# Kernel optimization log

Measured on AMD Instinct MI355X. Metric: run time of the kernel, lower is better.

The kernel has to match this reference:

```python
import jax, jax.numpy as jnp
import numpy as np

N_NODES = 100000
N_EDGES = 640000
IN_DIM, HID_DIM, OUT_DIM = 128, 64, 32


def setup_inputs() -> dict:
    key = jax.random.key(0)
    ks = jax.random.split(key, 8)
    x = jax.random.normal(ks[0], (N_NODES, IN_DIM), dtype=jnp.float32)
    edge_index = jax.random.randint(ks[1], (2, N_EDGES), 0, N_NODES, dtype=jnp.int64)
    # SAGEConv params: lin_l (applied to aggregated neighbors, has bias),
    # lin_r (applied to root node, no bias) -- PyG defaults.
    s1 = 1.0 / np.sqrt(IN_DIM)
    s2 = 1.0 / np.sqrt(HID_DIM)
    W1l = jax.random.uniform(ks[2], (HID_DIM, IN_DIM), jnp.float32, -s1, s1)
    b1 = jax.random.uniform(ks[3], (HID_DIM,), jnp.float32, -s1, s1)
    W1r = jax.random.uniform(ks[4], (HID_DIM, IN_DIM), jnp.float32, -s1, s1)
    W2l = jax.random.uniform(ks[5], (OUT_DIM, HID_DIM), jnp.float32, -s2, s2)
    b2 = jax.random.uniform(ks[6], (OUT_DIM,), jnp.float32, -s2, s2)
    W2r = jax.random.uniform(ks[7], (OUT_DIM, HID_DIM), jnp.float32, -s2, s2)
    return {"x": x, "edge_index": edge_index,
            "W1l": W1l, "b1": b1, "W1r": W1r,
            "W2l": W2l, "b2": b2, "W2r": W2r}


def _sage_conv(x, src, dst, Wl, b, Wr, num_nodes):
    # mean aggregation of source features onto destination nodes
    msg = x[src]                                                # [E, d]
    agg = jax.ops.segment_sum(msg, dst, num_segments=num_nodes)  # [N, d]
    cnt = jax.ops.segment_sum(jnp.ones((src.shape[0],), x.dtype), dst,
                              num_segments=num_nodes)            # [N]
    agg = agg / jnp.maximum(cnt, 1.0)[:, None]
    # out = lin_l(mean_neighbors) + lin_r(x)
    return agg @ Wl.T + b + x @ Wr.T


def reference(x, edge_index, W1l, b1, W1r, W2l, b2, W2r):
    src, dst = edge_index[0], edge_index[1]
    n = x.shape[0]
    h = jax.nn.relu(_sage_conv(x, src, dst, W1l, b1, W1r, n))
    out = _sage_conv(h, src, dst, W2l, b2, W2r, n)
    return out
```

## Files before the change

kernel.cpp:

```cpp
#include <hip/hip_runtime.h>
#include <hip/hip_bf16.h>

typedef __hip_bfloat16 bf16;
typedef __attribute__((ext_vector_type(8))) short short8;
typedef __attribute__((ext_vector_type(4))) float f32x4;

#define N_NODES 100000
#define N_EDGES 640000
#define NSB 98
#define N_TILES 6250

__device__ __forceinline__ int detect_is64(const int* __restrict__ idx) {
    int lane = threadIdx.x & 63;
    int v = idx[2 * (lane & 31) + 1];
    return __ballot(v == 0) == ~0ULL;
}
__device__ __forceinline__ int detect_f32(const unsigned* __restrict__ xw) {
    int lane = threadIdx.x & 63;
    unsigned e = (xw[lane] >> 7) & 0xFFu;
    int inr = (e >= 0x20u && e <= 0x4Fu);
    return __popcll(__ballot(inr)) < 48;
}

__device__ __forceinline__ void decode8(
        const int* __restrict__ eidx, int is64, int e0, int E,
        int (&ss)[8], int (&dd)[8]) {
    if (is64) {
        int4 a0 = *(const int4*)&eidx[2 * e0];
        int4 a1 = *(const int4*)&eidx[2 * e0 + 4];
        int4 a2 = *(const int4*)&eidx[2 * e0 + 8];
        int4 a3 = *(const int4*)&eidx[2 * e0 + 12];
        int4 b0 = *(const int4*)&eidx[2 * (E + e0)];
        int4 b1 = *(const int4*)&eidx[2 * (E + e0) + 4];
        int4 b2 = *(const int4*)&eidx[2 * (E + e0) + 8];
        int4 b3 = *(const int4*)&eidx[2 * (E + e0) + 12];
        ss[0] = a0.x; ss[1] = a0.z; ss[2] = a1.x; ss[3] = a1.z;
        ss[4] = a2.x; ss[5] = a2.z; ss[6] = a3.x; ss[7] = a3.z;
        dd[0] = b0.x; dd[1] = b0.z; dd[2] = b1.x; dd[3] = b1.z;
        dd[4] = b2.x; dd[5] = b2.z; dd[6] = b3.x; dd[7] = b3.z;
    } else {
        int4 s0 = *(const int4*)&eidx[e0];
        int4 s1 = *(const int4*)&eidx[e0 + 4];
        int4 d0 = *(const int4*)&eidx[E + e0];
        int4 d1 = *(const int4*)&eidx[E + e0 + 4];
        ss[0] = s0.x; ss[1] = s0.y; ss[2] = s0.z; ss[3] = s0.w;
        ss[4] = s1.x; ss[5] = s1.y; ss[6] = s1.z; ss[7] = s1.w;
        dd[0] = d0.x; dd[1] = d0.y; dd[2] = d0.z; dd[3] = d0.w;
        dd[4] = d1.x; dd[5] = d1.y; dd[6] = d1.z; dd[7] = d1.w;
    }
}

__global__ __launch_bounds__(256) void hist_kernel(
        const int* __restrict__ eidx, int* __restrict__ deg,
        int* __restrict__ rank, int E, int N) {
    const int is64 = detect_is64(eidx);
    int e0 = (blockIdx.x * 256 + threadIdx.x) * 8;
    if (e0 >= E) return;
    int ss[8], dd[8], rk[8];
    decode8(eidx, is64, e0, E, ss, dd);
#pragma unroll
    for (int c = 0; c < 8; ++c) {
        bool ok = (unsigned)ss[c] < (unsigned)N && (unsigned)dd[c] < (unsigned)N;
        rk[c] = ok ? atomicAdd(&deg[dd[c]], 1) : 0;
    }
    *(int4*)&rank[e0]     = make_int4(rk[0], rk[1], rk[2], rk[3]);
    *(int4*)&rank[e0 + 4] = make_int4(rk[4], rk[5], rk[6], rk[7]);
}

__global__ __launch_bounds__(256) void scan_partial_kernel(
        const int* __restrict__ deg, int* __restrict__ off,
        int* __restrict__ bsum, int N) {
    __shared__ int ss[256];
    const int tid = threadIdx.x, blk = blockIdx.x;
    const int base = blk * 1024 + tid * 4;
    int v[4], s = 0;
    if (base + 3 < N) {
        int4 dv = *(const int4*)&deg[base];
        v[0] = dv.x; v[1] = dv.y; v[2] = dv.z; v[3] = dv.w;
    } else {
#pragma unroll
        for (int c = 0; c < 4; ++c) v[c] = (base + c < N) ? deg[base + c] : 0;
    }
#pragma unroll
    for (int c = 0; c < 4; ++c) s += v[c];
    ss[tid] = s; __syncthreads();
    for (int o = 1; o < 256; o <<= 1) {
        int t = (tid >= o) ? ss[tid - o] : 0;
        __syncthreads();
        ss[tid] += t;
        __syncthreads();
    }
    int run = ss[tid] - s;
    if (tid == 255) bsum[blk] = ss[255];
#pragma unroll
    for (int c = 0; c < 4; ++c) {
        if (base + c < N) off[base + c] = run;
        run += v[c];
    }
}

__global__ void scan_bsum_kernel(int* __restrict__ bsum, int* __restrict__ off, int N) {
    __shared__ int ss[128];
    const int tid = threadIdx.x;
    int v = (tid < NSB) ? bsum[tid] : 0;
    ss[tid] = v; __syncthreads();
    for (int o = 1; o < 128; o <<= 1) {
        int t = (tid >= o) ? ss[tid - o] : 0;
        __syncthreads();
        ss[tid] += t;
        __syncthreads();
    }
    if (tid < NSB) bsum[tid] = ss[tid] - v;
    if (tid == 127) off[N] = ss[127];
}

__global__ __launch_bounds__(256) void scan_add_kernel(
        int* __restrict__ off, const int* __restrict__ bsum, int N) {
    const int blk = blockIdx.x, tid = threadIdx.x;
    const int add = bsum[blk];
    const int base = blk * 1024 + tid * 4;
#pragma unroll
    for (int c = 0; c < 4; ++c) {
        int i = base + c;
        if (i < N) off[i] += add;
    }
}

__global__ __launch_bounds__(256) void fill_kernel(
        const int* __restrict__ eidx, const int* __restrict__ off,
        const int* __restrict__ rank, int* __restrict__ srcs, int E, int N) {
    const int is64 = detect_is64(eidx);
    int e0 = (blockIdx.x * 256 + threadIdx.x) * 8;
    if (e0 >= E) return;
    int ss[8], dd[8];
    decode8(eidx, is64, e0, E, ss, dd);
    int4 r0 = *(const int4*)&rank[e0];
    int4 r1 = *(const int4*)&rank[e0 + 4];
    const int rk[8] = {r0.x, r0.y, r0.z, r0.w, r1.x, r1.y, r1.z, r1.w};
#pragma unroll
    for (int c = 0; c < 8; ++c) {
        if ((unsigned)ss[c] >= (unsigned)N || (unsigned)dd[c] >= (unsigned)N) continue;
        srcs[off[dd[c]] + rk[c]] = ss[c];
    }
}

__global__ __launch_bounds__(256) void gather1_kernel(
        const int* __restrict__ srcs, const int* __restrict__ off,
        const bf16* __restrict__ xl, const bf16* __restrict__ xr,
        const void* __restrict__ b1, bf16* __restrict__ h,
        const unsigned* __restrict__ xdet, int N) {
    const int f32 = detect_f32(xdet);
    const int node = blockIdx.x * 4 + (threadIdx.x >> 6);
    const int lane = threadIdx.x & 63;
    if (node >= N) return;
    const int a = off[node], b = off[node + 1];
    float acc = 0.f;
    for (int base = a; base < b; base += 64) {
        const int cdeg = min(b - base, 64);
        int sv = (lane < cdeg) ? srcs[base + lane] : 0;
        for (int bb = 0; bb < cdeg; bb += 8) {
            float v[8];
#pragma unroll
            for (int t = 0; t < 8; ++t) {
                int idx = bb + t;
                int s = __shfl(sv, idx < cdeg ? idx : 0);
                float val = (float)xl[(size_t)s * 64 + lane];
                v[t] = (idx < cdeg) ? val : 0.f;
            }
            acc += ((v[0] + v[1]) + (v[2] + v[3])) + ((v[4] + v[5]) + (v[6] + v[7]));
        }
    }
    const float bb = f32 ? ((const float*)b1)[lane] : (float)((const bf16*)b1)[lane];
    const float inv = 1.0f / fmaxf((float)(b - a), 1.0f);
    float v = acc * inv + bb + (float)xr[(size_t)node * 64 + lane];
    h[(size_t)node * 64 + lane] = __float2bfloat16(fmaxf(v, 0.0f));
}

__global__ __launch_bounds__(256) void gather2_kernel(
        const int* __restrict__ srcs, const int* __restrict__ off,
        const bf16* __restrict__ hl, const bf16* __restrict__ hr,
        const void* __restrict__ b2, void* __restrict__ out,
        const unsigned* __restrict__ xdet, int N) {
    const int f32 = detect_f32(xdet);
    const int node = blockIdx.x * 4 + (threadIdx.x >> 6);
    const int lane = threadIdx.x & 63;
    if (node >= N) return;
    const int j = lane & 31, half = lane >> 5;
    const int a = off[node], b = off[node + 1];
    float acc = 0.f;
    for (int base = a; base < b; base += 64) {
        const int cdeg = min(b - base, 64);
        int sv = (lane < cdeg) ? srcs[base + lane] : 0;
        for (int bb = 0; bb < cdeg; bb += 8) {
            float v[4];
#pragma unroll
            for (int t = 0; t < 4; ++t) {
                int idx = bb + half + 2 * t;
                int s = __shfl(sv, idx < cdeg ? idx : 0);
                float val = (float)hl[(size_t)s * 32 + j];
                v[t] = (idx < cdeg) ? val : 0.f;
            }
            acc += (v[0] + v[1]) + (v[2] + v[3]);
        }
    }
    acc += __shfl_down(acc, 32);
    if (half == 0) {
        const float bb = f32 ? ((const float*)b2)[j] : (float)((const bf16*)b2)[j];
        const float inv = 1.0f / fmaxf((float)(b - a), 1.0f);
        float v = acc * inv + bb + (float)hr[(size_t)node * 32 + j];
        if (f32) ((float*)out)[(size_t)node * 32 + j] = v;
        else     ((bf16*)out)[(size_t)node * 32 + j] = __float2bfloat16(v);
    }
}

__device__ __forceinline__ short8 load_frag(const void* base, size_t eoff, int f32) {
    if (f32) {
        const float4* p = (const float4*)((const float*)base + eoff);
        const float4 u = p[0], v = p[1];
        short8 r;
        union { bf16 b; short s; } t;
        t.b = __float2bfloat16(u.x); r[0] = t.s;
        t.b = __float2bfloat16(u.y); r[1] = t.s;
        t.b = __float2bfloat16(u.z); r[2] = t.s;
        t.b = __float2bfloat16(u.w); r[3] = t.s;
        t.b = __float2bfloat16(v.x); r[4] = t.s;
        t.b = __float2bfloat16(v.y); r[5] = t.s;
        t.b = __float2bfloat16(v.z); r[6] = t.s;
        t.b = __float2bfloat16(v.w); r[7] = t.s;
        return r;
    }
    return *(const short8*)((const short*)base + eoff);
}

__global__ __launch_bounds__(256) void lin1_kernel(
        const void* __restrict__ x, const void* __restrict__ W1l,
        const void* __restrict__ W1r, bf16* __restrict__ xl,
        bf16* __restrict__ xr) {
    const int f32 = detect_f32((const unsigned*)x);
    __shared__ short wlds[2][16][64][8];

    const int tid = threadIdx.x;
    {
        const int l = tid & 63, fg = tid >> 6;
        const int mm = l & 15, qq = l >> 4;
#pragma unroll
        for (int i = 0; i < 4; ++i) {
            const int f = fg * 4 + i;
            const int ks = f >> 2, nt = f & 3;
            const size_t wo = (size_t)(nt * 16 + mm) * 128 + ks * 32 + qq * 8;
            *(short8*)&wlds[0][f][l][0] = load_frag(W1l, wo, f32);
            *(short8*)&wlds[1][f][l][0] = load_frag(W1r, wo, f32);
        }
    }
    __syncthreads();

    const int nwaves = gridDim.x * 4;
    const int wid = blockIdx.x * 4 + (tid >> 6);
    const int lane = tid & 63;
    const int m = lane & 15, quad = lane >> 4;
    const short* wl0 = &wlds[0][0][lane][0];
    const short* wr0 = &wlds[1][0][lane][0];

    int tile = wid;
    if (tile >= N_TILES) return;

    short8 a[4];
    {
        const size_t arow = (size_t)(tile * 16 + m) * 128 + quad * 8;
#pragma unroll
        for (int ks = 0; ks < 4; ++ks)
            a[ks] = load_frag(x, arow + ks * 32, f32);
    }

    while (true) {
        const int nxt = tile + nwaves;
        short8 an[4];
        if (nxt < N_TILES) {
            const size_t arow = (size_t)(nxt * 16 + m) * 128 + quad * 8;
#pragma unroll
            for (int ks = 0; ks < 4; ++ks)
                an[ks] = load_frag(x, arow + ks * 32, f32);
        }

        f32x4 accl[4], accr[4];
#pragma unroll
        for (int nt = 0; nt < 4; ++nt) {
            accl[nt] = (f32x4){0.f, 0.f, 0.f, 0.f};
            accr[nt] = (f32x4){0.f, 0.f, 0.f, 0.f};
        }
#pragma unroll
        for (int ks = 0; ks < 4; ++ks)
#pragma unroll
            for (int nt = 0; nt < 4; ++nt) {
                const short8 wl = *(const short8*)(wl0 + (ks * 4 + nt) * 512);
                const short8 wr = *(const short8*)(wr0 + (ks * 4 + nt) * 512);
                accl[nt] = __builtin_amdgcn_mfma_f32_16x16x32_bf16(
                    a[ks], wl, accl[nt], 0, 0, 0);
                accr[nt] = __builtin_amdgcn_mfma_f32_16x16x32_bf16(
                    a[ks], wr, accr[nt], 0, 0, 0);
            }

        const int row0 = tile * 16;
#pragma unroll
        for (int reg = 0; reg < 4; ++reg) {
            const int row = row0 + quad * 4 + reg;
#pragma unroll
            for (int nt = 0; nt < 4; ++nt) {
                xl[(size_t)row * 64 + nt * 16 + m] = __float2bfloat16(accl[nt][reg]);
                xr[(size_t)row * 64 + nt * 16 + m] = __float2bfloat16(accr[nt][reg]);
            }
        }

        if (nxt >= N_TILES) break;
        tile = nxt;
#pragma unroll
        for (int ks = 0; ks < 4; ++ks) a[ks] = an[ks];
    }
}

__global__ __launch_bounds__(256) void lin2_kernel(
        const bf16* __restrict__ h, const void* __restrict__ W2l,
        const void* __restrict__ W2r, bf16* __restrict__ hl,
        bf16* __restrict__ hr, const unsigned* __restrict__ xdet) {
    const int f32 = detect_f32(xdet);
    const int nwaves = gridDim.x * 4;
    const int wid = blockIdx.x * 4 + (threadIdx.x >> 6);
    const int lane = threadIdx.x & 63;
    const int m = lane & 15, quad = lane >> 4;

    short8 bfr[8];
#pragma unroll
    for (int ks = 0; ks < 2; ++ks)
#pragma unroll
        for (int nt = 0; nt < 4; ++nt) {
            const void* Wb = (nt < 2) ? W2l : W2r;
            bfr[ks * 4 + nt] =
                load_frag(Wb, (size_t)((nt & 1) * 16 + m) * 64 + ks * 32 + quad * 8, f32);
        }

    for (int tile = wid; tile < N_TILES; tile += nwaves) {
        const int row0 = tile * 16;
        f32x4 acc[4];
#pragma unroll
        for (int nt = 0; nt < 4; ++nt) acc[nt] = (f32x4){0.f, 0.f, 0.f, 0.f};

        const size_t arow = (size_t)(row0 + m) * 64;
        short8 a[2];
#pragma unroll
        for (int ks = 0; ks < 2; ++ks)
            a[ks] = *(const short8*)((const short*)h + arow + ks * 32 + quad * 8);
#pragma unroll
        for (int ks = 0; ks < 2; ++ks)
#pragma unroll
            for (int nt = 0; nt < 4; ++nt)
                acc[nt] = __builtin_amdgcn_mfma_f32_16x16x32_bf16(
                    a[ks], bfr[ks * 4 + nt], acc[nt], 0, 0, 0);

#pragma unroll
        for (int reg = 0; reg < 4; ++reg) {
            const int row = row0 + quad * 4 + reg;
#pragma unroll
            for (int nt = 0; nt < 4; ++nt) {
                bf16* dst = (nt < 2) ? hl : hr;
                dst[(size_t)row * 32 + (nt & 1) * 16 + m] = __float2bfloat16(acc[nt][reg]);
            }
        }
    }
}

extern "C" void kernel_launch(void* const* d_in, const int* in_sizes, int n_in,
                              void* d_out, int out_size, void* d_ws, size_t ws_size,
                              hipStream_t stream) {
    const void* x   = d_in[0];
    const int*  eix = (const int*)d_in[1];
    const void* W1l = d_in[2];
    const void* b1  = d_in[3];
    const void* W1r = d_in[4];
    const void* W2l = d_in[5];
    const void* b2  = d_in[6];
    const void* W2r = d_in[7];

    const int N = N_NODES;
    const int E = N_EDGES;

    char* ws = (char*)d_ws;
    bf16*  xl    = (bf16*)(ws + 256);
    bf16*  xr    = (bf16*)(ws + 256 + (size_t)N * 128);
    bf16*  h     = (bf16*)(ws + 256 + (size_t)N * 256);
    bf16*  hl    = (bf16*)(ws + 256 + (size_t)N * 384);
    bf16*  hr    = (bf16*)(ws + 256 + (size_t)N * 448);
    int*   off   = (int*) (ws + 256 + (size_t)N * 512);
    int*   deg   = off + (N + 4);
    int*   rank  = deg + N;
    int*   srcs  = rank + E;
    int*   bsum  = srcs + E;

    hipMemsetAsync(deg, 0, (size_t)N * 4, stream);
    const int ge = (E / 8 + 255) / 256;
    hist_kernel<<<ge, 256, 0, stream>>>(eix, deg, rank, E, N);
    scan_partial_kernel<<<NSB, 256, 0, stream>>>(deg, off, bsum, N);
    scan_bsum_kernel<<<1, 128, 0, stream>>>(bsum, off, N);
    scan_add_kernel<<<NSB, 256, 0, stream>>>(off, bsum, N);
    fill_kernel<<<ge, 256, 0, stream>>>(eix, off, rank, srcs, E, N);

    const int gg = 782;

    lin1_kernel<<<gg, 256, 0, stream>>>(x, W1l, W1r, xl, xr);

    gather1_kernel<<<(N + 3) / 4, 256, 0, stream>>>(
        srcs, off, xl, xr, b1, h, (const unsigned*)x, N);

    lin2_kernel<<<gg, 256, 0, stream>>>(h, W2l, W2r, hl, hr, (const unsigned*)x);

    gather2_kernel<<<(N + 3) / 4, 256, 0, stream>>>(
        srcs, off, hl, hr, b2, d_out, (const unsigned*)x, N);
}
```

Before: 249.0 us.

## Vectorize gathers with sub-wave node groups, fuse scan pass, transpose MFMA outputs

The gather kernels now give each node a group of 16 (layer 1) or 8 (layer 2) lanes. Each lane loads four bf16 features as a short4, so more nodes are handled per wave and every load is wider. The single-block bsum scan kernel is removed, and each scan_add block now sums the preceding block totals itself. The MFMA operands in lin1 and lin2 are swapped so each lane holds four contiguous output columns of one node, which allows short4 stores instead of scattered 2-byte writes. Grid sizes also change, and the node bounds checks are dropped because the grids divide N exactly.

```diff
diff --git a/kernel.cpp b/kernel.cpp
--- a/kernel.cpp
+++ b/kernel.cpp
@@ -9,6 +9,17 @@
 #define N_EDGES 640000
 #define NSB 98
 #define N_TILES 6250
+
+__device__ __forceinline__ float bf2f(short s) {
+    union { float f; unsigned u; } u;
+    u.u = ((unsigned)(unsigned short)s) << 16;
+    return u.f;
+}
+__device__ __forceinline__ short f2s(float f) {
+    union { bf16 b; short s; } u;
+    u.b = __float2bfloat16(f);
+    return u.s;
+}
 
 __device__ __forceinline__ int detect_is64(const int* __restrict__ idx) {
     int lane = threadIdx.x & 63;
@@ -99,31 +110,22 @@
     }
 }
 
-__global__ void scan_bsum_kernel(int* __restrict__ bsum, int* __restrict__ off, int N) {
-    __shared__ int ss[128];
-    const int tid = threadIdx.x;
-    int v = (tid < NSB) ? bsum[tid] : 0;
-    ss[tid] = v; __syncthreads();
-    for (int o = 1; o < 128; o <<= 1) {
-        int t = (tid >= o) ? ss[tid - o] : 0;
-        __syncthreads();
-        ss[tid] += t;
-        __syncthreads();
-    }
-    if (tid < NSB) bsum[tid] = ss[tid] - v;
-    if (tid == 127) off[N] = ss[127];
-}
-
 __global__ __launch_bounds__(256) void scan_add_kernel(
         int* __restrict__ off, const int* __restrict__ bsum, int N) {
+    __shared__ int ss[NSB];
     const int blk = blockIdx.x, tid = threadIdx.x;
-    const int add = bsum[blk];
+    if (tid < NSB) ss[tid] = bsum[tid];
+    __syncthreads();
+    int add = 0;
+    for (int i = 0; i < blk; ++i) add += ss[i];
     const int base = blk * 1024 + tid * 4;
 #pragma unroll
     for (int c = 0; c < 4; ++c) {
         int i = base + c;
         if (i < N) off[i] += add;
     }
+    if (blk == NSB - 1 && tid == 0)
+        off[N] = add + ss[NSB - 1];
 }
 
 __global__ __launch_bounds__(256) void fill_kernel(
@@ -150,30 +152,44 @@
         const void* __restrict__ b1, bf16* __restrict__ h,
         const unsigned* __restrict__ xdet, int N) {
     const int f32 = detect_f32(xdet);
-    const int node = blockIdx.x * 4 + (threadIdx.x >> 6);
-    const int lane = threadIdx.x & 63;
-    if (node >= N) return;
+    const int tid = threadIdx.x;
+    const int node = blockIdx.x * 16 + (tid >> 4);
+    const int j = tid & 15;
+    const int gbase = (tid & 63) & ~15;
     const int a = off[node], b = off[node + 1];
-    float acc = 0.f;
-    for (int base = a; base < b; base += 64) {
-        const int cdeg = min(b - base, 64);
-        int sv = (lane < cdeg) ? srcs[base + lane] : 0;
-        for (int bb = 0; bb < cdeg; bb += 8) {
-            float v[8];
-#pragma unroll
-            for (int t = 0; t < 8; ++t) {
-                int idx = bb + t;
-                int s = __shfl(sv, idx < cdeg ? idx : 0);
-                float val = (float)xl[(size_t)s * 64 + lane];
-                v[t] = (idx < cdeg) ? val : 0.f;
+    float a0 = 0.f, a1 = 0.f, a2 = 0.f, a3 = 0.f;
+    for (int base = a; base < b; base += 16) {
+        const int cdeg = min(b - base, 16);
+        int sv = (j < cdeg) ? srcs[base + j] : 0;
+        for (int bb = 0; bb < cdeg; bb += 4) {
+#pragma unroll
+            for (int t = 0; t < 4; ++t) {
+                const int idx = bb + t;
+                const int s = __shfl(sv, gbase + (idx < cdeg ? idx : 0));
+                if (idx < cdeg) {
+                    short4 v = *(const short4*)((const short*)xl + (size_t)s * 64 + j * 4);
+                    a0 += bf2f(v.x); a1 += bf2f(v.y);
+                    a2 += bf2f(v.z); a3 += bf2f(v.w);
+                }
             }
-            acc += ((v[0] + v[1]) + (v[2] + v[3])) + ((v[4] + v[5]) + (v[6] + v[7]));
-        }
-    }
-    const float bb = f32 ? ((const float*)b1)[lane] : (float)((const bf16*)b1)[lane];
+        }
+    }
+    float b0, b1v, b2v, b3;
+    if (f32) {
+        float4 bb4 = *(const float4*)((const float*)b1 + j * 4);
+        b0 = bb4.x; b1v = bb4.y; b2v = bb4.z; b3 = bb4.w;
+    } else {
+        short4 bb4 = *(const short4*)((const short*)b1 + j * 4);
+        b0 = bf2f(bb4.x); b1v = bf2f(bb4.y); b2v = bf2f(bb4.z); b3 = bf2f(bb4.w);
+    }
+    short4 xr4 = *(const short4*)((const short*)xr + (size_t)node * 64 + j * 4);
     const float inv = 1.0f / fmaxf((float)(b - a), 1.0f);
-    float v = acc * inv + bb + (float)xr[(size_t)node * 64 + lane];
-    h[(size_t)node * 64 + lane] = __float2bfloat16(fmaxf(v, 0.0f));
+    short4 o;
+    o.x = f2s(fmaxf(a0 * inv + b0  + bf2f(xr4.x), 0.0f));
+    o.y = f2s(fmaxf(a1 * inv + b1v + bf2f(xr4.y), 0.0f));
+    o.z = f2s(fmaxf(a2 * inv + b2v + bf2f(xr4.z), 0.0f));
+    o.w = f2s(fmaxf(a3 * inv + b3  + bf2f(xr4.w), 0.0f));
+    *(short4*)((short*)h + (size_t)node * 64 + j * 4) = o;
 }
 
 __global__ __launch_bounds__(256) void gather2_kernel(
@@ -182,34 +198,49 @@
         const void* __restrict__ b2, void* __restrict__ out,
         const unsigned* __restrict__ xdet, int N) {
     const int f32 = detect_f32(xdet);
-    const int node = blockIdx.x * 4 + (threadIdx.x >> 6);
-    const int lane = threadIdx.x & 63;
-    if (node >= N) return;
-    const int j = lane & 31, half = lane >> 5;
+    const int tid = threadIdx.x;
+    const int node = blockIdx.x * 32 + (tid >> 3);
+    const int j = tid & 7;
+    const int gbase = (tid & 63) & ~7;
     const int a = off[node], b = off[node + 1];
-    float acc = 0.f;
-    for (int base = a; base < b; base += 64) {
-        const int cdeg = min(b - base, 64);
-        int sv = (lane < cdeg) ? srcs[base + lane] : 0;
-        for (int bb = 0; bb < cdeg; bb += 8) {
-            float v[4];
+    float a0 = 0.f, a1 = 0.f, a2 = 0.f, a3 = 0.f;
+    for (int base = a; base < b; base += 8) {
+        const int cdeg = min(b - base, 8);
+        int sv = (j < cdeg) ? srcs[base + j] : 0;
+        for (int bb = 0; bb < cdeg; bb += 4) {
 #pragma unroll
             for (int t = 0; t < 4; ++t) {
-                int idx = bb + half + 2 * t;
-                int s = __shfl(sv, idx < cdeg ? idx : 0);
-                float val = (float)hl[(size_t)s * 32 + j];
-                v[t] = (idx < cdeg) ? val : 0.f;
+                const int idx = bb + t;
+                const int s = __shfl(sv, gbase + (idx < cdeg ? idx : 0));
+                if (idx < cdeg) {
+                    short4 v = *(const short4*)((const short*)hl + (size_t)s * 32 + j * 4);
+                    a0 += bf2f(v.x); a1 += bf2f(v.y);
+                    a2 += bf2f(v.z); a3 += bf2f(v.w);
+                }
             }
-            acc += (v[0] + v[1]) + (v[2] + v[3]);
-        }
-    }
-    acc += __shfl_down(acc, 32);
-    if (half == 0) {
-        const float bb = f32 ? ((const float*)b2)[j] : (float)((const bf16*)b2)[j];
-        const float inv = 1.0f / fmaxf((float)(b - a), 1.0f);
-        float v = acc * inv + bb + (float)hr[(size_t)node * 32 + j];
-        if (f32) ((float*)out)[(size_t)node * 32 + j] = v;
-        else     ((bf16*)out)[(size_t)node * 32 + j] = __float2bfloat16(v);
+        }
+    }
+    float b0, b1v, b2v, b3;
+    if (f32) {
+        float4 bb4 = *(const float4*)((const float*)b2 + j * 4);
+        b0 = bb4.x; b1v = bb4.y; b2v = bb4.z; b3 = bb4.w;
+    } else {
+        short4 bb4 = *(const short4*)((const short*)b2 + j * 4);
+        b0 = bf2f(bb4.x); b1v = bf2f(bb4.y); b2v = bf2f(bb4.z); b3 = bf2f(bb4.w);
+    }
+    short4 hr4 = *(const short4*)((const short*)hr + (size_t)node * 32 + j * 4);
+    const float inv = 1.0f / fmaxf((float)(b - a), 1.0f);
+    const float v0 = a0 * inv + b0  + bf2f(hr4.x);
+    const float v1 = a1 * inv + b1v + bf2f(hr4.y);
+    const float v2 = a2 * inv + b2v + bf2f(hr4.z);
+    const float v3 = a3 * inv + b3  + bf2f(hr4.w);
+    if (f32) {
+        *(float4*)((float*)out + (size_t)node * 32 + j * 4) =
+            make_float4(v0, v1, v2, v3);
+    } else {
+        short4 o;
+        o.x = f2s(v0); o.y = f2s(v1); o.z = f2s(v2); o.w = f2s(v3);
+        *(short4*)((short*)out + (size_t)node * 32 + j * 4) = o;
     }
 }
 
@@ -218,15 +249,8 @@
         const float4* p = (const float4*)((const float*)base + eoff);
         const float4 u = p[0], v = p[1];
         short8 r;
-        union { bf16 b; short s; } t;
-        t.b = __float2bfloat16(u.x); r[0] = t.s;
-        t.b = __float2bfloat16(u.y); r[1] = t.s;
-        t.b = __float2bfloat16(u.z); r[2] = t.s;
-        t.b = __float2bfloat16(u.w); r[3] = t.s;
-        t.b = __float2bfloat16(v.x); r[4] = t.s;
-        t.b = __float2bfloat16(v.y); r[5] = t.s;
-        t.b = __float2bfloat16(v.z); r[6] = t.s;
-        t.b = __float2bfloat16(v.w); r[7] = t.s;
+        r[0] = f2s(u.x); r[1] = f2s(u.y); r[2] = f2s(u.z); r[3] = f2s(u.w);
+        r[4] = f2s(v.x); r[5] = f2s(v.y); r[6] = f2s(v.z); r[7] = f2s(v.w);
         return r;
     }
     return *(const short8*)((const short*)base + eoff);
@@ -246,8 +270,8 @@
 #pragma unroll
         for (int i = 0; i < 4; ++i) {
             const int f = fg * 4 + i;
-            const int ks = f >> 2, nt = f & 3;
-            const size_t wo = (size_t)(nt * 16 + mm) * 128 + ks * 32 + qq * 8;
+            const int ks = f >> 2, dt = f & 3;
+            const size_t wo = (size_t)(dt * 16 + mm) * 128 + ks * 32 + qq * 8;
             *(short8*)&wlds[0][f][l][0] = load_frag(W1l, wo, f32);
             *(short8*)&wlds[1][f][l][0] = load_frag(W1r, wo, f32);
         }
@@ -284,31 +308,32 @@
 
         f32x4 accl[4], accr[4];
 #pragma unroll
-        for (int nt = 0; nt < 4; ++nt) {
-            accl[nt] = (f32x4){0.f, 0.f, 0.f, 0.f};
-            accr[nt] = (f32x4){0.f, 0.f, 0.f, 0.f};
+        for (int dt = 0; dt < 4; ++dt) {
+            accl[dt] = (f32x4){0.f, 0.f, 0.f, 0.f};
+            accr[dt] = (f32x4){0.f, 0.f, 0.f, 0.f};
         }
 #pragma unroll
         for (int ks = 0; ks < 4; ++ks)
 #pragma unroll
-            for (int nt = 0; nt < 4; ++nt) {
-                const short8 wl = *(const short8*)(wl0 + (ks * 4 + nt) * 512);
-                const short8 wr = *(const short8*)(wr0 + (ks * 4 + nt) * 512);
-                accl[nt] = __builtin_amdgcn_mfma_f32_16x16x32_bf16(
-                    a[ks], wl, accl[nt], 0, 0, 0);
-                accr[nt] = __builtin_amdgcn_mfma_f32_16x16x32_bf16(
-                    a[ks], wr, accr[nt], 0, 0, 0);
+            for (int dt = 0; dt < 4; ++dt) {
+                const short8 wl = *(const short8*)(wl0 + (ks * 4 + dt) * 512);
+                const short8 wr = *(const short8*)(wr0 + (ks * 4 + dt) * 512);
+                accl[dt] = __builtin_amdgcn_mfma_f32_16x16x32_bf16(
+                    wl, a[ks], accl[dt], 0, 0, 0);
+                accr[dt] = __builtin_amdgcn_mfma_f32_16x16x32_bf16(
+                    wr, a[ks], accr[dt], 0, 0, 0);
             }
 
-        const int row0 = tile * 16;
-#pragma unroll
-        for (int reg = 0; reg < 4; ++reg) {
-            const int row = row0 + quad * 4 + reg;
-#pragma unroll
-            for (int nt = 0; nt < 4; ++nt) {
-                xl[(size_t)row * 64 + nt * 16 + m] = __float2bfloat16(accl[nt][reg]);
-                xr[(size_t)row * 64 + nt * 16 + m] = __float2bfloat16(accr[nt][reg]);
-            }
+        const int node = tile * 16 + m;
+#pragma unroll
+        for (int dt = 0; dt < 4; ++dt) {
+            short4 pl, pr;
+            pl.x = f2s(accl[dt][0]); pl.y = f2s(accl[dt][1]);
+            pl.z = f2s(accl[dt][2]); pl.w = f2s(accl[dt][3]);
+            pr.x = f2s(accr[dt][0]); pr.y = f2s(accr[dt][1]);
+            pr.z = f2s(accr[dt][2]); pr.w = f2s(accr[dt][3]);
+            *(short4*)((short*)xl + (size_t)node * 64 + dt * 16 + quad * 4) = pl;
+            *(short4*)((short*)xr + (size_t)node * 64 + dt * 16 + quad * 4) = pr;
         }
 
         if (nxt >= N_TILES) break;
@@ -339,12 +364,11 @@
         }
 
     for (int tile = wid; tile < N_TILES; tile += nwaves) {
-        const int row0 = tile * 16;
         f32x4 acc[4];
 #pragma unroll
         for (int nt = 0; nt < 4; ++nt) acc[nt] = (f32x4){0.f, 0.f, 0.f, 0.f};
 
-        const size_t arow = (size_t)(row0 + m) * 64;
+        const size_t arow = (size_t)(tile * 16 + m) * 64;
         short8 a[2];
 #pragma unroll
         for (int ks = 0; ks < 2; ++ks)
@@ -354,16 +378,16 @@
 #pragma unroll
             for (int nt = 0; nt < 4; ++nt)
                 acc[nt] = __builtin_amdgcn_mfma_f32_16x16x32_bf16(
-                    a[ks], bfr[ks * 4 + nt], acc[nt], 0, 0, 0);
-
-#pragma unroll
-        for (int reg = 0; reg < 4; ++reg) {
-            const int row = row0 + quad * 4 + reg;
-#pragma unroll
-            for (int nt = 0; nt < 4; ++nt) {
-                bf16* dst = (nt < 2) ? hl : hr;
-                dst[(size_t)row * 32 + (nt & 1) * 16 + m] = __float2bfloat16(acc[nt][reg]);
-            }
+                    bfr[ks * 4 + nt], a[ks], acc[nt], 0, 0, 0);
+
+        const int node = tile * 16 + m;
+#pragma unroll
+        for (int nt = 0; nt < 4; ++nt) {
+            bf16* dst = (nt < 2) ? hl : hr;
+            short4 p;
+            p.x = f2s(acc[nt][0]); p.y = f2s(acc[nt][1]);
+            p.z = f2s(acc[nt][2]); p.w = f2s(acc[nt][3]);
+            *(short4*)((short*)dst + (size_t)node * 32 + (nt & 1) * 16 + quad * 4) = p;
         }
     }
 }
@@ -399,19 +423,16 @@
     const int ge = (E / 8 + 255) / 256;
     hist_kernel<<<ge, 256, 0, stream>>>(eix, deg, rank, E, N);
     scan_partial_kernel<<<NSB, 256, 0, stream>>>(deg, off, bsum, N);
-    scan_bsum_kernel<<<1, 128, 0, stream>>>(bsum, off, N);
     scan_add_kernel<<<NSB, 256, 0, stream>>>(off, bsum, N);
     fill_kernel<<<ge, 256, 0, stream>>>(eix, off, rank, srcs, E, N);
 
-    const int gg = 782;
-
-    lin1_kernel<<<gg, 256, 0, stream>>>(x, W1l, W1r, xl, xr);
-
-    gather1_kernel<<<(N + 3) / 4, 256, 0, stream>>>(
+    lin1_kernel<<<1024, 256, 0, stream>>>(x, W1l, W1r, xl, xr);
+
+    gather1_kernel<<<N / 16, 256, 0, stream>>>(
         srcs, off, xl, xr, b1, h, (const unsigned*)x, N);
 
-    lin2_kernel<<<gg, 256, 0, stream>>>(h, W2l, W2r, hl, hr, (const unsigned*)x);
-
-    gather2_kernel<<<(N + 3) / 4, 256, 0, stream>>>(
+    lin2_kernel<<<1024, 256, 0, stream>>>(h, W2l, W2r, hl, hr, (const unsigned*)x);
+
+    gather2_kernel<<<N / 32, 256, 0, stream>>>(
         srcs, off, hl, hr, b2, d_out, (const unsigned*)x, N);
 }
```

New measurement: 220.8 us. -11.3%, faster.
